# Performance work log

Measured on AMD Instinct MI355X. Metric: run time of the kernel, lower is better.

Reference implementation:

```python
import jax, jax.numpy as jnp
import numpy as np

B, IN, H = 8192, 1024, 1024


def setup_inputs() -> dict:
    key = jax.random.key(0)
    ks = jax.random.split(key, 6)
    s = 1.0 / np.sqrt(H)
    return {
        "incoming": jax.random.normal(ks[0], (B, IN), dtype=jnp.float32),
        "state": jax.random.normal(ks[1], (2, B, H), dtype=jnp.float32),
        "Wx": jax.random.normal(ks[2], (4 * H, IN), dtype=jnp.float32) * s,
        "bx": jax.random.normal(ks[3], (4 * H,), dtype=jnp.float32) * s,
        "Wh": jax.random.normal(ks[4], (4 * H, H), dtype=jnp.float32) * s,
        "bh": jax.random.normal(ks[5], (4 * H,), dtype=jnp.float32) * s,
    }


def reference(incoming, state, Wx, bx, Wh, bh):
    # Fused form of 8 Linear layers: gates stacked in (i, f, g, o) order.
    h_prev, c_prev = state[0], state[1]
    gates = (jnp.einsum('bi,gi->bg', incoming, Wx) + bx
             + jnp.einsum('bh,gh->bg', h_prev, Wh) + bh)  # [B, 4H]
    i_g, f_g, g_g, o_g = jnp.split(gates, 4, axis=-1)
    i = jax.nn.sigmoid(i_g)
    f = jax.nn.sigmoid(f_g)
    g = jnp.tanh(g_g)
    o = jax.nn.sigmoid(o_g)
    new_c = f * c_prev + i * g
    new_h = o * jnp.tanh(new_c)
    # output == new_h; return stacked (new_h, new_c) as [2, B, H]
    return jnp.stack([new_h, new_c])
```

## Files before the change

### kernel.cpp

```cpp
#include <hip/hip_runtime.h>
#include <hip/hip_bf16.h>


#define B_DIM 8192
#define H_DIM 1024
#define BH (8192 * 1024)
#define K2 2048

typedef __attribute__((ext_vector_type(4))) float f32x4;
typedef __attribute__((ext_vector_type(8))) __bf16 bf16x8;
typedef __attribute__((ext_vector_type(8))) unsigned short ushort8;

static __device__ __forceinline__ unsigned short f2bf(float f) {
    return __builtin_bit_cast(unsigned short, (__bf16)f);
}
static __device__ __forceinline__ float sigf(float x) {
    return 1.0f / (1.0f + __expf(-x));
}
static __device__ __forceinline__ float tanhft(float x) {
    float e = __expf(2.0f * x);
    return (e - 1.0f) / (e + 1.0f);
}
static __device__ __forceinline__ void gload16(const void* g, void* l) {
    __builtin_amdgcn_global_load_lds(
        (const __attribute__((address_space(1))) unsigned int*)g,
        (__attribute__((address_space(3))) unsigned int*)l, 16, 0, 0);
}
static __device__ __forceinline__ ushort8 cvt8(const float* src) {
    const float4 u = ((const float4*)src)[0];
    const float4 v = ((const float4*)src)[1];
    ushort8 o;
    o[0] = f2bf(u.x); o[1] = f2bf(u.y); o[2] = f2bf(u.z); o[3] = f2bf(u.w);
    o[4] = f2bf(v.x); o[5] = f2bf(v.y); o[6] = f2bf(v.z); o[7] = f2bf(v.w);
    return o;
}

__global__ __launch_bounds__(256) void conv_kernel(
    const float* __restrict__ x, const float* __restrict__ h,
    const float* __restrict__ Wx, const float* __restrict__ Wh,
    unsigned short* __restrict__ A, unsigned short* __restrict__ W)
{
    const int bidx = blockIdx.x;
    if (bidx < 8192) {
        const int id = bidx * 256 + threadIdx.x;
        const int base = id * 8;
        const int b = base >> 11;
        const int k = base & 2047;
        const float* src = (k < 1024) ? (x + (size_t)b * 1024 + k)
                                      : (h + (size_t)b * 1024 + (k - 1024));
        *(ushort8*)(A + base) = cvt8(src);
    } else {
        const int id = (bidx - 8192) * 256 + threadIdx.x;
        const int base = id * 8;
        const int n = base >> 11;
        const int k = base & 2047;
        const int jb = n >> 8, wn = (n >> 6) & 3, g = (n >> 4) & 3, jj = n & 15;
        const int srow = (g << 10) + (jb << 6) + (wn << 4) + jj;
        const float* src = (k < 1024) ? (Wx + (size_t)srow * 1024 + k)
                                      : (Wh + (size_t)srow * 1024 + (k - 1024));
        *(ushort8*)(W + base) = cvt8(src);
    }
}

__global__ __launch_bounds__(1024, 4) void lstm_gemm8(
    const unsigned short* __restrict__ Abf, const unsigned short* __restrict__ Wbf,
    const float* __restrict__ bx, const float* __restrict__ bh,
    const float* __restrict__ cprev, float* __restrict__ out)
{
    extern __shared__ unsigned short lds[];

    const int tid = threadIdx.x;
    const int lane = tid & 63;
    const int wv = tid >> 6;
    const int wm = wv >> 2;
    const int wn = wv & 3;
    const int q = lane >> 4, c = lane & 15;

    const int bid = blockIdx.x;
    const int xcd = bid & 7;
    const int idx = bid >> 3;
    const int jb  = xcd * 2 + (idx & 1);
    const int bb  = idx >> 1;
    const int b0 = bb * 256;

    const unsigned short* Ab = Abf + (size_t)b0 * K2;
    const unsigned short* Wb = Wbf + (size_t)(jb * 256) * K2;

    const size_t ssg = (size_t)(tid >> 2) * K2
                     + (size_t)(((tid & 3) ^ ((tid >> 3) & 3)) * 8);
    const unsigned sdst = (unsigned)(tid & 960) * 8;

    const unsigned cq = (unsigned)((q ^ ((c >> 1) & 3)) << 3);
    const unsigned arow = (unsigned)(wm * 64 + c) * 32 + cq;
    const unsigned brow = 8192u + (unsigned)(wn * 64 + c) * 32 + cq;

    f32x4 acc[4][4];
#pragma unroll
    for (int m = 0; m < 4; ++m)
#pragma unroll
        for (int g = 0; g < 4; ++g) acc[m][g] = f32x4{0.f, 0.f, 0.f, 0.f};

    bf16x8 av[4], bv[4];

#define STG(BUF, ISB, T) do {                                                  \
    const unsigned short* _s = (ISB) ? Wb : Ab;                                \
    gload16(_s + ssg + (size_t)((T) & 63) * 32,                                \
            &lds[(BUF) * 16384 + (ISB) * 8192 + sdst]);                        \
} while (0)

#define RD(BUF) do {                                                           \
    const unsigned short* _pa = lds + (BUF) * 16384 + arow;                    \
    const unsigned short* _pb = lds + (BUF) * 16384 + brow;                    \
    av[0] = *(const bf16x8*)(_pa);                                             \
    av[1] = *(const bf16x8*)(_pa + 512);                                       \
    av[2] = *(const bf16x8*)(_pa + 1024);                                      \
    av[3] = *(const bf16x8*)(_pa + 1536);                                      \
    bv[0] = *(const bf16x8*)(_pb);                                             \
    bv[1] = *(const bf16x8*)(_pb + 512);                                       \
    bv[2] = *(const bf16x8*)(_pb + 1024);                                      \
    bv[3] = *(const bf16x8*)(_pb + 1536);                                      \
} while (0)

#define MFMA16() do {                                                          \
    __builtin_amdgcn_s_setprio(1);                                             \
    _Pragma("unroll")                                                          \
    for (int _i = 0; _i < 4; ++_i)                                             \
        _Pragma("unroll")                                                      \
        for (int _g = 0; _g < 4; ++_g)                                         \
            acc[_i][_g] = __builtin_amdgcn_mfma_f32_16x16x32_bf16(             \
                av[_i], bv[_g], acc[_i][_g], 0, 0, 0);                         \
    __builtin_amdgcn_s_setprio(0);                                             \
} while (0)

#define BAR()  __builtin_amdgcn_s_barrier()
#define WVM0() asm volatile("s_waitcnt vmcnt(0)" ::: "memory")

#define KTILE(BUF, T1) do {                                                    \
    STG((BUF) ^ 1, 0, T1);                                                     \
    STG((BUF) ^ 1, 1, T1);                                                     \
    RD(BUF);                                                                   \
    MFMA16();                                                                  \
    WVM0();                                                                    \
    BAR();                                                                     \
} while (0)

    STG(0, 0, 0); STG(0, 1, 0);
    WVM0();
    BAR();

    for (int t = 0; t < 64; t += 2) {
        KTILE(0, t + 1);
        KTILE(1, t + 2);
    }

#undef KTILE
#undef STG
#undef RD
#undef MFMA16

    const int j = jb * 64 + wn * 16 + c;
    const float bI = bx[j] + bh[j];
    const float bF = bx[1024 + j] + bh[1024 + j];
    const float bG = bx[2048 + j] + bh[2048 + j];
    const float bO = bx[3072 + j] + bh[3072 + j];
#pragma unroll
    for (int mt = 0; mt < 4; ++mt) {
#pragma unroll
        for (int rr = 0; rr < 4; ++rr) {
            const int row = b0 + wm * 64 + mt * 16 + q * 4 + rr;
            const size_t off = (size_t)row * 1024 + j;
            const float iv = sigf(acc[mt][0][rr] + bI);
            const float fv = sigf(acc[mt][1][rr] + bF);
            const float gv = tanhft(acc[mt][2][rr] + bG);
            const float ov = sigf(acc[mt][3][rr] + bO);
            const float cp = cprev[off];
            const float nc = fv * cp + iv * gv;
            out[off] = ov * tanhft(nc);
            out[BH + off] = nc;
        }
    }
}

__global__ __launch_bounds__(256) void lstm_fallback(
    const float* __restrict__ incoming, const float* __restrict__ state,
    const float* __restrict__ Wx, const float* __restrict__ bx,
    const float* __restrict__ Wh, const float* __restrict__ bh,
    float* __restrict__ out)
{
    __shared__ unsigned short lA[128 * 64];
    __shared__ unsigned short lW[128 * 64];
    const int t = threadIdx.x;
    const int lane = t & 63;
    const int wv = t >> 6;
    const int q = lane >> 4;
    const int c = lane & 15;
    const int j0 = blockIdx.x * 32;
    const int b0 = blockIdx.y * 128;
    const float* hprev = state;
    const float* cprev = state + (size_t)BH;

    f32x4 acc[2][8];
#pragma unroll
    for (int mt = 0; mt < 2; ++mt)
#pragma unroll
        for (int nt = 0; nt < 8; ++nt)
            acc[mt][nt] = f32x4{0.f, 0.f, 0.f, 0.f};

    const int sr = t >> 3;
    const int sk8 = t & 7;

    for (int it = 0; it < 32; ++it) {
        const bool first = (it < 16);
        const float* As = first ? incoming : hprev;
        const float* Ws = first ? Wx : Wh;
        const int kk = first ? it * 64 : it * 64 - 1024;
#pragma unroll
        for (int i = 0; i < 4; ++i) {
            const int r = i * 32 + sr;
            *(ushort8*)&lA[r * 64 + ((sk8 ^ (r & 7)) * 8)] =
                cvt8(As + (size_t)(b0 + r) * 1024 + kk + sk8 * 8);
        }
#pragma unroll
        for (int i = 0; i < 4; ++i) {
            const int n = i * 32 + sr;
            const int grow = ((n >> 5) << 10) + j0 + (n & 31);
            *(ushort8*)&lW[n * 64 + ((sk8 ^ (n & 7)) * 8)] =
                cvt8(Ws + (size_t)grow * 1024 + kk + sk8 * 8);
        }
        __syncthreads();
#pragma unroll
        for (int ks = 0; ks < 2; ++ks) {
            const int k8a = ks * 4 + q;
            bf16x8 av[2], bv[8];
#pragma unroll
            for (int mt = 0; mt < 2; ++mt) {
                const int r = wv * 32 + mt * 16 + c;
                av[mt] = *(const bf16x8*)&lA[r * 64 + ((k8a ^ (r & 7)) * 8)];
            }
#pragma unroll
            for (int nt = 0; nt < 8; ++nt) {
                const int n = nt * 16 + c;
                bv[nt] = *(const bf16x8*)&lW[n * 64 + ((k8a ^ (n & 7)) * 8)];
            }
#pragma unroll
            for (int mt = 0; mt < 2; ++mt)
#pragma unroll
                for (int nt = 0; nt < 8; ++nt)
                    acc[mt][nt] = __builtin_amdgcn_mfma_f32_16x16x32_bf16(
                        av[mt], bv[nt], acc[mt][nt], 0, 0, 0);
        }
        __syncthreads();
    }

    const int b0r = b0 + wv * 32;
#pragma unroll
    for (int jt = 0; jt < 2; ++jt) {
        const int j = j0 + jt * 16 + c;
        const float bI = bx[j] + bh[j];
        const float bF = bx[1024 + j] + bh[1024 + j];
        const float bG = bx[2048 + j] + bh[2048 + j];
        const float bO = bx[3072 + j] + bh[3072 + j];
#pragma unroll
        for (int mt = 0; mt < 2; ++mt) {
#pragma unroll
            for (int rr = 0; rr < 4; ++rr) {
                const int row = b0r + mt * 16 + q * 4 + rr;
                const size_t off = (size_t)row * 1024 + j;
                const float iv = sigf(acc[mt][0 + jt][rr] + bI);
                const float fv = sigf(acc[mt][2 + jt][rr] + bF);
                const float gv = tanhft(acc[mt][4 + jt][rr] + bG);
                const float ov = sigf(acc[mt][6 + jt][rr] + bO);
                const float cp = cprev[off];
                const float nc = fv * cp + iv * gv;
                out[off] = ov * tanhft(nc);
                out[BH + off] = nc;
            }
        }
    }
}

extern "C" void kernel_launch(void* const* d_in, const int* in_sizes, int n_in,
                              void* d_out, int out_size, void* d_ws, size_t ws_size,
                              hipStream_t stream) {
    const float* incoming = (const float*)d_in[0];
    const float* state    = (const float*)d_in[1];
    const float* Wx       = (const float*)d_in[2];
    const float* bx       = (const float*)d_in[3];
    const float* Wh       = (const float*)d_in[4];
    const float* bh       = (const float*)d_in[5];
    float* out = (float*)d_out;

    const float* hprev = state;
    const float* cprev = state + (size_t)BH;

    const size_t A_bytes = (size_t)B_DIM * K2 * 2;
    const size_t W_bytes = (size_t)4 * H_DIM * K2 * 2;

    if (ws_size >= A_bytes + W_bytes) {
        unsigned short* Abf = (unsigned short*)d_ws;
        unsigned short* Wbf = (unsigned short*)((char*)d_ws + A_bytes);
        conv_kernel<<<dim3(12288), dim3(256), 0, stream>>>(
            incoming, hprev, Wx, Wh, Abf, Wbf);
        (void)hipFuncSetAttribute((const void*)lstm_gemm8,
                                  hipFuncAttributeMaxDynamicSharedMemorySize, 65536);
        lstm_gemm8<<<dim3(512), dim3(1024), 65536, stream>>>(
            Abf, Wbf, bx, bh, cprev, out);
    } else {
        dim3 grid(H_DIM / 32, B_DIM / 128);
        lstm_fallback<<<grid, dim3(256), 0, stream>>>(
            incoming, state, Wx, bx, Wh, bh, out);
    }
}
```

Before: 165.0 us.

## Retile LSTM GEMM to 256x128 blocks with 4 waves and deeper prefetch

Replaces the 1024-thread, 256x256-tile GEMM with 256-thread blocks computing 256 batch rows by 128 gate columns. Each wave now holds a 128x64 accumulator tile (8x4 MFMA fragments), which raises per-wave register reuse. The weight permutation in the conversion kernel is rewritten to match the new 32-unit column grouping. The pipeline now keeps two tiles in flight with a partial vmcnt wait, aiming to hide global-to-LDS latency. The cost is higher register pressure per wave and more per-thread load instructions.

Result: slower. 178.6 us (+8.3%).

```diff
diff --git a/kernel.cpp b/kernel.cpp
--- a/kernel.cpp
+++ b/kernel.cpp
@@ -54,15 +54,16 @@
         const int base = id * 8;
         const int n = base >> 11;
         const int k = base & 2047;
-        const int jb = n >> 8, wn = (n >> 6) & 3, g = (n >> 4) & 3, jj = n & 15;
-        const int srow = (g << 10) + (jb << 6) + (wn << 4) + jj;
+        const int jb = n >> 7, loc = n & 127;
+        const int g = loc >> 5, wn = (loc >> 4) & 1, jj = loc & 15;
+        const int srow = (g << 10) + (jb << 5) + (wn << 4) + jj;
         const float* src = (k < 1024) ? (Wx + (size_t)srow * 1024 + k)
                                       : (Wh + (size_t)srow * 1024 + (k - 1024));
         *(ushort8*)(W + base) = cvt8(src);
     }
 }
 
-__global__ __launch_bounds__(1024, 4) void lstm_gemm8(
+__global__ __launch_bounds__(256, 2) void lstm_gemm(
     const unsigned short* __restrict__ Abf, const unsigned short* __restrict__ Wbf,
     const float* __restrict__ bx, const float* __restrict__ bh,
     const float* __restrict__ cprev, float* __restrict__ out)
@@ -72,59 +73,67 @@
     const int tid = threadIdx.x;
     const int lane = tid & 63;
     const int wv = tid >> 6;
-    const int wm = wv >> 2;
-    const int wn = wv & 3;
+    const int wm = wv >> 1;
+    const int wn = wv & 1;
     const int q = lane >> 4, c = lane & 15;
 
     const int bid = blockIdx.x;
     const int xcd = bid & 7;
     const int idx = bid >> 3;
-    const int jb  = xcd * 2 + (idx & 1);
-    const int bb  = idx >> 1;
+    const int jb  = xcd * 4 + (idx & 3);
+    const int bb  = idx >> 2;
     const int b0 = bb * 256;
 
     const unsigned short* Ab = Abf + (size_t)b0 * K2;
-    const unsigned short* Wb = Wbf + (size_t)(jb * 256) * K2;
+    const unsigned short* Wb = Wbf + (size_t)(jb * 128) * K2;
 
     const size_t ssg = (size_t)(tid >> 2) * K2
                      + (size_t)(((tid & 3) ^ ((tid >> 3) & 3)) * 8);
-    const unsigned sdst = (unsigned)(tid & 960) * 8;
-
-    const unsigned cq = (unsigned)((q ^ ((c >> 1) & 3)) << 3);
-    const unsigned arow = (unsigned)(wm * 64 + c) * 32 + cq;
-    const unsigned brow = 8192u + (unsigned)(wn * 64 + c) * 32 + cq;
-
-    f32x4 acc[4][4];
-#pragma unroll
-    for (int m = 0; m < 4; ++m)
+    const unsigned sdA = (unsigned)(tid & 192) * 8;
+
+    const unsigned cqa = (unsigned)((q ^ ((c >> 1) & 3)) << 3);
+    const unsigned aBase = (unsigned)(wm * 128 + c) * 32 + cqa;
+    const unsigned bBase = 8192u + (unsigned)(wn * 16 + c) * 32 + cqa;
+
+    f32x4 acc[8][4];
+#pragma unroll
+    for (int m = 0; m < 8; ++m)
 #pragma unroll
         for (int g = 0; g < 4; ++g) acc[m][g] = f32x4{0.f, 0.f, 0.f, 0.f};
 
-    bf16x8 av[4], bv[4];
-
-#define STG(BUF, ISB, T) do {                                                  \
-    const unsigned short* _s = (ISB) ? Wb : Ab;                                \
-    gload16(_s + ssg + (size_t)((T) & 63) * 32,                                \
-            &lds[(BUF) * 16384 + (ISB) * 8192 + sdst]);                        \
+    bf16x8 av[8], bv[4];
+
+#define STG(BUF, T) do {                                                       \
+    const size_t _t = (size_t)((T) & 63) * 32;                                 \
+    gload16(Ab + ssg + _t,                &lds[(BUF) * 12288 + sdA]);          \
+    gload16(Ab + ssg + (size_t)64 * K2 + _t,  &lds[(BUF) * 12288 + 2048 + sdA]);\
+    gload16(Ab + ssg + (size_t)128 * K2 + _t, &lds[(BUF) * 12288 + 4096 + sdA]);\
+    gload16(Ab + ssg + (size_t)192 * K2 + _t, &lds[(BUF) * 12288 + 6144 + sdA]);\
+    gload16(Wb + ssg + _t,                &lds[(BUF) * 12288 + 8192 + sdA]);   \
+    gload16(Wb + ssg + (size_t)64 * K2 + _t, &lds[(BUF) * 12288 + 10240 + sdA]);\
 } while (0)
 
 #define RD(BUF) do {                                                           \
-    const unsigned short* _pa = lds + (BUF) * 16384 + arow;                    \
-    const unsigned short* _pb = lds + (BUF) * 16384 + brow;                    \
+    const unsigned short* _pa = lds + (BUF) * 12288 + aBase;                   \
+    const unsigned short* _pb = lds + (BUF) * 12288 + bBase;                   \
+    bv[0] = *(const bf16x8*)(_pb);                                             \
+    bv[1] = *(const bf16x8*)(_pb + 1024);                                      \
+    bv[2] = *(const bf16x8*)(_pb + 2048);                                      \
+    bv[3] = *(const bf16x8*)(_pb + 3072);                                      \
     av[0] = *(const bf16x8*)(_pa);                                             \
     av[1] = *(const bf16x8*)(_pa + 512);                                       \
     av[2] = *(const bf16x8*)(_pa + 1024);                                      \
     av[3] = *(const bf16x8*)(_pa + 1536);                                      \
-    bv[0] = *(const bf16x8*)(_pb);                                             \
-    bv[1] = *(const bf16x8*)(_pb + 512);                                       \
-    bv[2] = *(const bf16x8*)(_pb + 1024);                                      \
-    bv[3] = *(const bf16x8*)(_pb + 1536);                                      \
+    av[4] = *(const bf16x8*)(_pa + 2048);                                      \
+    av[5] = *(const bf16x8*)(_pa + 2560);                                      \
+    av[6] = *(const bf16x8*)(_pa + 3072);                                      \
+    av[7] = *(const bf16x8*)(_pa + 3584);                                      \
 } while (0)
 
-#define MFMA16() do {                                                          \
+#define MFMA32() do {                                                          \
     __builtin_amdgcn_s_setprio(1);                                             \
     _Pragma("unroll")                                                          \
-    for (int _i = 0; _i < 4; ++_i)                                             \
+    for (int _i = 0; _i < 8; ++_i)                                             \
         _Pragma("unroll")                                                      \
         for (int _g = 0; _g < 4; ++_g)                                         \
             acc[_i][_g] = __builtin_amdgcn_mfma_f32_16x16x32_bf16(             \
@@ -133,41 +142,41 @@
 } while (0)
 
 #define BAR()  __builtin_amdgcn_s_barrier()
-#define WVM0() asm volatile("s_waitcnt vmcnt(0)" ::: "memory")
-
-#define KTILE(BUF, T1) do {                                                    \
-    STG((BUF) ^ 1, 0, T1);                                                     \
-    STG((BUF) ^ 1, 1, T1);                                                     \
+#define WVM6() asm volatile("s_waitcnt vmcnt(6)" ::: "memory")
+
+#define KTILE(BUF, T2) do {                                                    \
     RD(BUF);                                                                   \
-    MFMA16();                                                                  \
-    WVM0();                                                                    \
+    MFMA32();                                                                  \
+    BAR();                                                                     \
+    STG(BUF, T2);                                                              \
+    WVM6();                                                                    \
     BAR();                                                                     \
 } while (0)
 
-    STG(0, 0, 0); STG(0, 1, 0);
-    WVM0();
+    STG(0, 0); STG(1, 1);
+    WVM6();
     BAR();
 
     for (int t = 0; t < 64; t += 2) {
-        KTILE(0, t + 1);
-        KTILE(1, t + 2);
+        KTILE(0, t + 2);
+        KTILE(1, t + 3);
     }
 
 #undef KTILE
 #undef STG
 #undef RD
-#undef MFMA16
-
-    const int j = jb * 64 + wn * 16 + c;
+#undef MFMA32
+
+    const int j = jb * 32 + wn * 16 + c;
     const float bI = bx[j] + bh[j];
     const float bF = bx[1024 + j] + bh[1024 + j];
     const float bG = bx[2048 + j] + bh[2048 + j];
     const float bO = bx[3072 + j] + bh[3072 + j];
 #pragma unroll
-    for (int mt = 0; mt < 4; ++mt) {
+    for (int mt = 0; mt < 8; ++mt) {
 #pragma unroll
         for (int rr = 0; rr < 4; ++rr) {
-            const int row = b0 + wm * 64 + mt * 16 + q * 4 + rr;
+            const int row = b0 + wm * 128 + mt * 16 + q * 4 + rr;
             const size_t off = (size_t)row * 1024 + j;
             const float iv = sigf(acc[mt][0][rr] + bI);
             const float fv = sigf(acc[mt][1][rr] + bF);
@@ -301,9 +310,9 @@
         unsigned short* Wbf = (unsigned short*)((char*)d_ws + A_bytes);
         conv_kernel<<<dim3(12288), dim3(256), 0, stream>>>(
             incoming, hprev, Wx, Wh, Abf, Wbf);
-        (void)hipFuncSetAttribute((const void*)lstm_gemm8,
-                                  hipFuncAttributeMaxDynamicSharedMemorySize, 65536);
-        lstm_gemm8<<<dim3(512), dim3(1024), 65536, stream>>>(
+        (void)hipFuncSetAttribute((const void*)lstm_gemm,
+                                  hipFuncAttributeMaxDynamicSharedMemorySize, 49152);
+        lstm_gemm<<<dim3(1024), dim3(256), 49152, stream>>>(
             Abf, Wbf, bx, bh, cprev, out);
     } else {
         dim3 grid(H_DIM / 32, B_DIM / 128);
```

## Switch GEMM to 32x32x16 MFMA with 8 waves and split-K double buffering

Applied to the files above, without the earlier changes.

Replaces the 16x16x32 MFMA tiling with 32x32x16 bf16 MFMA. The block shrinks to 512 threads (8 waves in a 4x2 layout), each wave computing 64 batch rows by 32 columns for all four gates. Each k-step now stages 64 K per buffer in two 32-wide sub-phases with 128 KB of LDS, and partial vmcnt waits let loads overlap compute. The weight permutation in the conversion kernel is updated to match the new column-to-wave mapping. The aim is fewer LDS reads per FLOP and higher MFMA throughput, at the cost of lower occupancy and more barriers per tile.

Result: slower. 182.6 us (+10.7%).

```diff
diff --git a/kernel.cpp b/kernel.cpp
--- a/kernel.cpp
+++ b/kernel.cpp
@@ -8,6 +8,7 @@
 #define K2 2048
 
 typedef __attribute__((ext_vector_type(4))) float f32x4;
+typedef __attribute__((ext_vector_type(16))) float f32x16;
 typedef __attribute__((ext_vector_type(8))) __bf16 bf16x8;
 typedef __attribute__((ext_vector_type(8))) unsigned short ushort8;
 
@@ -54,15 +55,15 @@
         const int base = id * 8;
         const int n = base >> 11;
         const int k = base & 2047;
-        const int jb = n >> 8, wn = (n >> 6) & 3, g = (n >> 4) & 3, jj = n & 15;
-        const int srow = (g << 10) + (jb << 6) + (wn << 4) + jj;
+        const int jb = n >> 8, gate = (n >> 6) & 3, wn = (n >> 5) & 1, jcol = n & 31;
+        const int srow = (gate << 10) + (jb << 6) + (wn << 5) + jcol;
         const float* src = (k < 1024) ? (Wx + (size_t)srow * 1024 + k)
                                       : (Wh + (size_t)srow * 1024 + (k - 1024));
         *(ushort8*)(W + base) = cvt8(src);
     }
 }
 
-__global__ __launch_bounds__(1024, 4) void lstm_gemm8(
+__global__ __launch_bounds__(512, 2) void lstm_gemm32(
     const unsigned short* __restrict__ Abf, const unsigned short* __restrict__ Wbf,
     const float* __restrict__ bx, const float* __restrict__ bh,
     const float* __restrict__ cprev, float* __restrict__ out)
@@ -72,107 +73,119 @@
     const int tid = threadIdx.x;
     const int lane = tid & 63;
     const int wv = tid >> 6;
-    const int wm = wv >> 2;
-    const int wn = wv & 3;
-    const int q = lane >> 4, c = lane & 15;
+    const int wm = wv >> 1;
+    const int wn = wv & 1;
+    const int rl = lane & 31, hi = lane >> 5;
 
     const int bid = blockIdx.x;
     const int xcd = bid & 7;
     const int idx = bid >> 3;
     const int jb  = xcd * 2 + (idx & 1);
     const int bb  = idx >> 1;
-    const int b0 = bb * 256;
+    const int b0  = bb * 256;
 
     const unsigned short* Ab = Abf + (size_t)b0 * K2;
     const unsigned short* Wb = Wbf + (size_t)(jb * 256) * K2;
 
     const size_t ssg = (size_t)(tid >> 2) * K2
                      + (size_t)(((tid & 3) ^ ((tid >> 3) & 3)) * 8);
-    const unsigned sdst = (unsigned)(tid & 960) * 8;
-
-    const unsigned cq = (unsigned)((q ^ ((c >> 1) & 3)) << 3);
-    const unsigned arow = (unsigned)(wm * 64 + c) * 32 + cq;
-    const unsigned brow = 8192u + (unsigned)(wn * 64 + c) * 32 + cq;
-
-    f32x4 acc[4][4];
-#pragma unroll
-    for (int m = 0; m < 4; ++m)
-#pragma unroll
-        for (int g = 0; g < 4; ++g) acc[m][g] = f32x4{0.f, 0.f, 0.f, 0.f};
-
-    bf16x8 av[4], bv[4];
-
-#define STG(BUF, ISB, T) do {                                                  \
-    const unsigned short* _s = (ISB) ? Wb : Ab;                                \
-    gload16(_s + ssg + (size_t)((T) & 63) * 32,                                \
-            &lds[(BUF) * 16384 + (ISB) * 8192 + sdst]);                        \
+    const unsigned sd = (unsigned)(tid & 448) * 8;
+
+    const unsigned cs = (unsigned)((hi ^ ((rl >> 1) & 3)) << 3);
+    const unsigned aB = (unsigned)(wm * 64 + rl) * 32 + cs;
+    const unsigned wB = 16384u + (unsigned)(wn * 32 + rl) * 32 + cs;
+
+    f32x16 acc[2][4];
+#pragma unroll
+    for (int b_ = 0; b_ < 2; ++b_)
+#pragma unroll
+        for (int g_ = 0; g_ < 4; ++g_)
+#pragma unroll
+            for (int e_ = 0; e_ < 16; ++e_) acc[b_][g_][e_] = 0.f;
+
+    bf16x8 av[2][2], wf[4][2];
+
+#define STG4(BUF, KS, T) do {                                                  \
+    const size_t _t = (size_t)((T) & 31) * 64 + (KS) * 32;                     \
+    const unsigned _r = (BUF) * 32768u + (KS) * 8192u;                         \
+    gload16(Ab + ssg + _t,                    &lds[_r + sd]);                  \
+    gload16(Ab + ssg + (size_t)128 * K2 + _t, &lds[_r + 4096u + sd]);          \
+    gload16(Wb + ssg + _t,                    &lds[_r + 16384u + sd]);         \
+    gload16(Wb + ssg + (size_t)128 * K2 + _t, &lds[_r + 20480u + sd]);         \
 } while (0)
 
-#define RD(BUF) do {                                                           \
-    const unsigned short* _pa = lds + (BUF) * 16384 + arow;                    \
-    const unsigned short* _pb = lds + (BUF) * 16384 + brow;                    \
-    av[0] = *(const bf16x8*)(_pa);                                             \
-    av[1] = *(const bf16x8*)(_pa + 512);                                       \
-    av[2] = *(const bf16x8*)(_pa + 1024);                                      \
-    av[3] = *(const bf16x8*)(_pa + 1536);                                      \
-    bv[0] = *(const bf16x8*)(_pb);                                             \
-    bv[1] = *(const bf16x8*)(_pb + 512);                                       \
-    bv[2] = *(const bf16x8*)(_pb + 1024);                                      \
-    bv[3] = *(const bf16x8*)(_pb + 1536);                                      \
+#define RD12(BUF, KS) do {                                                     \
+    const unsigned short* _p = lds + (BUF) * 32768 + (KS) * 8192;              \
+    av[0][0] = *(const bf16x8*)&_p[aB];                                        \
+    av[1][0] = *(const bf16x8*)&_p[aB + 1024];                                 \
+    av[0][1] = *(const bf16x8*)&_p[aB ^ 16];                                   \
+    av[1][1] = *(const bf16x8*)&_p[(aB ^ 16) + 1024];                          \
+    wf[0][0] = *(const bf16x8*)&_p[wB];                                        \
+    wf[1][0] = *(const bf16x8*)&_p[wB + 2048];                                 \
+    wf[2][0] = *(const bf16x8*)&_p[wB + 4096];                                 \
+    wf[3][0] = *(const bf16x8*)&_p[wB + 6144];                                 \
+    wf[0][1] = *(const bf16x8*)&_p[wB ^ 16];                                   \
+    wf[1][1] = *(const bf16x8*)&_p[(wB ^ 16) + 2048];                          \
+    wf[2][1] = *(const bf16x8*)&_p[(wB ^ 16) + 4096];                          \
+    wf[3][1] = *(const bf16x8*)&_p[(wB ^ 16) + 6144];                          \
 } while (0)
 
-#define MFMA16() do {                                                          \
+#define MFMA16X() do {                                                         \
     __builtin_amdgcn_s_setprio(1);                                             \
     _Pragma("unroll")                                                          \
-    for (int _i = 0; _i < 4; ++_i)                                             \
+    for (int _k = 0; _k < 2; ++_k)                                             \
         _Pragma("unroll")                                                      \
-        for (int _g = 0; _g < 4; ++_g)                                         \
-            acc[_i][_g] = __builtin_amdgcn_mfma_f32_16x16x32_bf16(             \
-                av[_i], bv[_g], acc[_i][_g], 0, 0, 0);                         \
+        for (int _b = 0; _b < 2; ++_b)                                         \
+            _Pragma("unroll")                                                  \
+            for (int _g = 0; _g < 4; ++_g)                                     \
+                acc[_b][_g] = __builtin_amdgcn_mfma_f32_32x32x16_bf16(         \
+                    av[_b][_k], wf[_g][_k], acc[_b][_g], 0, 0, 0);             \
     __builtin_amdgcn_s_setprio(0);                                             \
 } while (0)
 
-#define BAR()  __builtin_amdgcn_s_barrier()
-#define WVM0() asm volatile("s_waitcnt vmcnt(0)" ::: "memory")
-
-#define KTILE(BUF, T1) do {                                                    \
-    STG((BUF) ^ 1, 0, T1);                                                     \
-    STG((BUF) ^ 1, 1, T1);                                                     \
-    RD(BUF);                                                                   \
-    MFMA16();                                                                  \
-    WVM0();                                                                    \
+#define BAR()    __builtin_amdgcn_s_barrier()
+#define WLGKM0() asm volatile("s_waitcnt lgkmcnt(0)")
+#define WVM4()   asm volatile("s_waitcnt vmcnt(4)" ::: "memory")
+
+#define PHASE(BUF, KS, T1) do {                                                \
+    RD12(BUF, KS);                                                             \
+    STG4((BUF) ^ 1, KS, T1);                                                   \
+    BAR();                                                                     \
+    WLGKM0();                                                                  \
+    MFMA16X();                                                                 \
+    WVM4();                                                                    \
     BAR();                                                                     \
 } while (0)
 
-    STG(0, 0, 0); STG(0, 1, 0);
-    WVM0();
+    STG4(0, 0, 0); STG4(0, 1, 0);
+    WVM4();
     BAR();
 
-    for (int t = 0; t < 64; t += 2) {
-        KTILE(0, t + 1);
-        KTILE(1, t + 2);
-    }
-
-#undef KTILE
-#undef STG
-#undef RD
-#undef MFMA16
-
-    const int j = jb * 64 + wn * 16 + c;
+    for (int t = 0; t < 32; t += 2) {
+        PHASE(0, 0, t + 1); PHASE(0, 1, t + 1);
+        PHASE(1, 0, t + 2); PHASE(1, 1, t + 2);
+    }
+
+#undef PHASE
+#undef STG4
+#undef RD12
+#undef MFMA16X
+
+    const int j = jb * 64 + wn * 32 + rl;
     const float bI = bx[j] + bh[j];
     const float bF = bx[1024 + j] + bh[1024 + j];
     const float bG = bx[2048 + j] + bh[2048 + j];
     const float bO = bx[3072 + j] + bh[3072 + j];
 #pragma unroll
-    for (int mt = 0; mt < 4; ++mt) {
-#pragma unroll
-        for (int rr = 0; rr < 4; ++rr) {
-            const int row = b0 + wm * 64 + mt * 16 + q * 4 + rr;
-            const size_t off = (size_t)row * 1024 + j;
-            const float iv = sigf(acc[mt][0][rr] + bI);
-            const float fv = sigf(acc[mt][1][rr] + bF);
-            const float gv = tanhft(acc[mt][2][rr] + bG);
-            const float ov = sigf(acc[mt][3][rr] + bO);
+    for (int bf = 0; bf < 2; ++bf) {
+#pragma unroll
+        for (int r = 0; r < 16; ++r) {
+            const int b = b0 + wm * 64 + bf * 32 + (r & 3) + 8 * (r >> 2) + 4 * hi;
+            const size_t off = (size_t)b * 1024 + j;
+            const float iv = sigf(acc[bf][0][r] + bI);
+            const float fv = sigf(acc[bf][1][r] + bF);
+            const float gv = tanhft(acc[bf][2][r] + bG);
+            const float ov = sigf(acc[bf][3][r] + bO);
             const float cp = cprev[off];
             const float nc = fv * cp + iv * gv;
             out[off] = ov * tanhft(nc);
@@ -301,9 +314,9 @@
         unsigned short* Wbf = (unsigned short*)((char*)d_ws + A_bytes);
         conv_kernel<<<dim3(12288), dim3(256), 0, stream>>>(
             incoming, hprev, Wx, Wh, Abf, Wbf);
-        (void)hipFuncSetAttribute((const void*)lstm_gemm8,
-                                  hipFuncAttributeMaxDynamicSharedMemorySize, 65536);
-        lstm_gemm8<<<dim3(512), dim3(1024), 65536, stream>>>(
+        (void)hipFuncSetAttribute((const void*)lstm_gemm32,
+                                  hipFuncAttributeMaxDynamicSharedMemorySize, 131072);
+        lstm_gemm32<<<dim3(512), dim3(512), 131072, stream>>>(
             Abf, Wbf, bx, bh, cprev, out);
     } else {
         dim3 grid(H_DIM / 32, B_DIM / 128);
```
